# Kernel tuning notes

Hardware: AMD Instinct MI355X
Metric: run time of the kernel (lower is better)

Reference implementation:

```python
import jax, jax.numpy as jnp
import numpy as np

BETA = 0.25  # commitment_beta


def setup_inputs() -> dict:
    key = jax.random.key(0)
    k1, k2 = jax.random.split(key)
    B, C, H, W = 8, 256, 32, 32
    n_embed = 16384
    x = jax.random.normal(k1, (B, C, H, W), dtype=jnp.float32)
    # torch init: uniform_(-1/codebook_size, 1/codebook_size)
    weight = jax.random.uniform(k2, (n_embed, C), dtype=jnp.float32,
                                minval=-1.0 / n_embed, maxval=1.0 / n_embed)
    return {"x": x, "weight": weight}


def reference(x, weight):
    B, C, H, W = x.shape
    # b c h w -> b (h w) c
    xf = jnp.transpose(x, (0, 2, 3, 1)).reshape(B, H * W, C)
    flat = xf.reshape(-1, C)  # [N, C], N = B*H*W
    d = (jnp.sum(flat * flat, axis=1, keepdims=True)
         + jnp.sum(weight * weight, axis=1)[None, :]
         - 2.0 * flat @ weight.T)
    idx = jnp.argmin(d, axis=-1)          # [N]
    xq = weight[idx].reshape(B, H * W, C)  # codebook gather
    sg = jax.lax.stop_gradient
    loss = (BETA * jnp.mean((sg(xq) - xf) ** 2)
            + jnp.mean((xq - sg(xf)) ** 2))
    # straight-through estimator
    xq_st = xf + sg(xq - xf)
    # b (h w) c -> b c h w
    xq_img = jnp.transpose(xq_st.reshape(B, H, W, C), (0, 3, 1, 2))
    x_code = idx.reshape(B, H, W)
    return xq_img, loss, x_code
```

## Files before the change

### kernel.cpp

```cpp
#include <hip/hip_runtime.h>
#include <stdint.h>

#define NROW    8192
#define CDIM    256
#define NCODE   16384
#define MARGINF 6.0e-5f

typedef short short8 __attribute__((ext_vector_type(8)));
typedef float floatx4 __attribute__((ext_vector_type(4)));

__device__ inline ushort f2bf(float f) {
    unsigned u = __builtin_bit_cast(unsigned, f);
    unsigned r = (u + 0x7fffu + ((u >> 16) & 1u)) >> 16;
    return (ushort)r;
}
__device__ inline unsigned fsort(float v) {
    unsigned u = __builtin_bit_cast(unsigned, v);
    return (u >> 31) ? ~u : (u | 0x80000000u);
}

__device__ inline void gl_lds16(const ushort* g, ushort* lds) {
    __builtin_amdgcn_global_load_lds(
        (const __attribute__((address_space(1))) unsigned int*)(g),
        (__attribute__((address_space(3))) unsigned int*)(lds),
        16, 0, 0);
}

__global__ __launch_bounds__(256) void prep_all(const float* __restrict__ x,
                                                const float* __restrict__ w,
                                                float* __restrict__ xf32,
                                                ushort* __restrict__ xbf,
                                                ushort* __restrict__ wbf,
                                                float* __restrict__ S2a) {
#pragma clang fp contract(off)
    const int bid = blockIdx.x;
    const int t = threadIdx.x;
    if (bid < 2048) {
        __shared__ float tile[32][33];
        const int b = bid & 7, ht = (bid >> 3) & 31, ct = bid >> 8;
        const int hw0 = ht * 32, c0 = ct * 32;
        {
            const int cc = t >> 5, hh = t & 31;
            #pragma unroll
            for (int i = 0; i < 4; ++i) {
                int cl = cc + i * 8;
                tile[cl][hh] = x[((size_t)(b * 256 + c0 + cl) << 10) + hw0 + hh];
            }
        }
        __syncthreads();
        {
            const int col = t & 31, row = t >> 5;
            #pragma unroll
            for (int i = 0; i < 4; ++i) {
                int r = row + i * 8;
                float v = tile[col][r];
                size_t o = ((size_t)(b * 1024 + hw0 + r) << 8) + c0 + col;
                xf32[o] = v;
                xbf[o] = f2bf(v);
            }
        }
    } else {
        const int gt = (bid - 2048) * 256 + t;
        const int j = gt >> 1, h = gt & 1;
        const float* a = w + ((size_t)j << 8) + h * 128;
        ushort* orow = wbf + ((size_t)j << 8) + h * 128;
        float r8[8];
        #pragma unroll
        for (int l = 0; l < 8; ++l) { float v = a[l]; r8[l] = v * v; }
        for (int i = 8; i < 128; i += 8) {
            #pragma unroll
            for (int l = 0; l < 8; ++l) { float v = a[i + l]; r8[l] = r8[l] + v * v; }
        }
        float hs = ((r8[0] + r8[1]) + (r8[2] + r8[3])) + ((r8[4] + r8[5]) + (r8[6] + r8[7]));
        float other = __shfl_xor(hs, 1);
        if (h == 0) S2a[j] = hs + other;
        for (int i = 0; i < 128; i += 8) {
            ushort u8[8];
            #pragma unroll
            for (int l = 0; l < 8; ++l) u8[l] = f2bf(a[i + l]);
            *(ushort4*)(orow + i)     = make_ushort4(u8[0], u8[1], u8[2], u8[3]);
            *(ushort4*)(orow + i + 4) = make_ushort4(u8[4], u8[5], u8[6], u8[7]);
        }
    }
}

__global__ __launch_bounds__(256) void gemm_min(const ushort* __restrict__ Wb,
                                                const ushort* __restrict__ Xb,
                                                const float* __restrict__ S2a,
                                                unsigned* __restrict__ bm32) {
    __shared__ __attribute__((aligned(16))) ushort As[8192];
    __shared__ __attribute__((aligned(16))) ushort Bs[8192];
    __shared__ __attribute__((aligned(16))) unsigned stg32[128][8];

    const int n0 = blockIdx.x * 128;
    const int j0 = blockIdx.y * 128;
    const int t  = threadIdx.x;
    const int wv = t >> 6, l = t & 63;
    const int wr = wv >> 1, wc = wv & 1;
    const int q  = l >> 4, c = l & 15;

    const int lr = l >> 3;
    const int lperm = (l & 7) ^ lr;
    const size_t gA0 = ((size_t)(j0 + wv * 32 + lr) << 8) + lperm * 8;
    const size_t gB0 = ((size_t)(n0 + wv * 32 + lr) << 8) + lperm * 8;
    const int ldsbase = wv * 2048;

    floatx4 acc[4][4];
    #pragma unroll
    for (int mi = 0; mi < 4; ++mi)
        #pragma unroll
        for (int ni = 0; ni < 4; ++ni)
            acc[mi][ni] = (floatx4){0.f, 0.f, 0.f, 0.f};

    for (int kb = 0; kb < 4; ++kb) {
        if (kb) __syncthreads();
        #pragma unroll
        for (int ca = 0; ca < 4; ++ca) {
            gl_lds16(Wb + gA0 + ca * 2048 + kb * 64, As + ldsbase + ca * 512);
            gl_lds16(Xb + gB0 + ca * 2048 + kb * 64, Bs + ldsbase + ca * 512);
        }
        __syncthreads();
        #pragma unroll
        for (int kk = 0; kk < 2; ++kk) {
            short8 af[4], bf[4];
            #pragma unroll
            for (int mi = 0; mi < 4; ++mi) {
                int row = wr * 64 + mi * 16 + c;
                int pos = (kk * 4 + q) ^ (c & 7);
                af[mi] = *(const short8*)&As[row * 64 + pos * 8];
            }
            #pragma unroll
            for (int ni = 0; ni < 4; ++ni) {
                int row = wc * 64 + ni * 16 + c;
                int pos = (kk * 4 + q) ^ (c & 7);
                bf[ni] = *(const short8*)&Bs[row * 64 + pos * 8];
            }
            #pragma unroll
            for (int mi = 0; mi < 4; ++mi)
                #pragma unroll
                for (int ni = 0; ni < 4; ++ni)
                    acc[mi][ni] = __builtin_amdgcn_mfma_f32_16x16x32_bf16(
                        af[mi], bf[ni], acc[mi][ni], 0, 0, 0);
        }
    }

    #pragma unroll
    for (int mi = 0; mi < 4; ++mi) {
        float4 s2 = *(const float4*)&S2a[j0 + wr * 64 + mi * 16 + (q << 2)];
        #pragma unroll
        for (int ni = 0; ni < 4; ++ni) {
            float v0 = fmaf(-2.f, acc[mi][ni][0], s2.x);
            float v1 = fmaf(-2.f, acc[mi][ni][1], s2.y);
            float v2 = fmaf(-2.f, acc[mi][ni][2], s2.z);
            float v3 = fmaf(-2.f, acc[mi][ni][3], s2.w);
            float lo01 = fminf(v0, v1), hi01 = fmaxf(v0, v1);
            float lo23 = fminf(v2, v3), hi23 = fmaxf(v2, v3);
            int   i01 = v1 < v0 ? 1 : 0;
            int   i23 = v3 < v2 ? 3 : 2;
            float m1 = fminf(lo01, lo23);
            float m2 = fminf(fmaxf(lo01, lo23), lo23 < lo01 ? hi23 : hi01);
            int   i1 = (q << 2) | (lo23 < lo01 ? i23 : i01);
            #pragma unroll
            for (int off = 16; off <= 32; off <<= 1) {
                float om1 = __shfl_xor(m1, off);
                float om2 = __shfl_xor(m2, off);
                int   oi1 = __shfl_xor(i1, off);
                float nm2 = fminf(fminf(m2, om2), fmaxf(m1, om1));
                i1 = om1 < m1 ? oi1 : i1;
                m1 = fminf(m1, om1);
                m2 = nm2;
            }
            if (q == 0) {
                ushort min16 = __builtin_bit_cast(ushort, (_Float16)m1);
                float delta = m2 - m1;
                ushort d16 = __builtin_bit_cast(ushort, (_Float16)delta);
                ushort d8 = d16 >> 8;
                float rec = (float)__builtin_bit_cast(_Float16, (ushort)(d8 << 8));
                if (rec > delta && d8) d8--;
                stg32[wc * 64 + ni * 16 + c][wr * 4 + mi] =
                    ((unsigned)min16 << 16) | ((unsigned)d8 << 8) | (unsigned)i1;
            }
        }
    }
    __syncthreads();
    if (t < 128) {
        uint4 a0 = *(const uint4*)&stg32[t][0];
        uint4 a1 = *(const uint4*)&stg32[t][4];
        size_t base = ((size_t)(n0 + t) << 10) + blockIdx.y * 8;
        *(uint4*)(bm32 + base)     = a0;
        *(uint4*)(bm32 + base + 4) = a1;
    }
}

__global__ __launch_bounds__(256) void rescore7(const unsigned* __restrict__ bm32,
                                                const float* __restrict__ xf32,
                                                const float* __restrict__ w,
                                                const float* __restrict__ S2a,
                                                int* __restrict__ idxb,
                                                float* __restrict__ xcode,
                                                float* __restrict__ lpart) {
#pragma clang fp contract(off)
    __shared__ float xs[4][256];
    __shared__ short sing[4][128];
    __shared__ short blk[4][32];
    __shared__ int ns[4], nb[4];

    const int t = threadIdx.x, wv = t >> 6, l = t & 63;
    const int n = blockIdx.x * 4 + wv;
    if (l == 0) { ns[wv] = 0; nb[wv] = 0; }

    const float4 xv = *(const float4*)&xf32[((size_t)n << 8) + l * 4];
    *(float4*)&xs[wv][l * 4] = xv;

    const unsigned* bp = bm32 + ((size_t)n << 10) + l * 16;
    unsigned ee[16];
    {
        uint4 e0 = *(const uint4*)(bp);
        uint4 e1 = *(const uint4*)(bp + 4);
        uint4 e2 = *(const uint4*)(bp + 8);
        uint4 e3 = *(const uint4*)(bp + 12);
        ee[0]=e0.x; ee[1]=e0.y; ee[2]=e0.z; ee[3]=e0.w;
        ee[4]=e1.x; ee[5]=e1.y; ee[6]=e1.z; ee[7]=e1.w;
        ee[8]=e2.x; ee[9]=e2.y; ee[10]=e2.z; ee[11]=e2.w;
        ee[12]=e3.x; ee[13]=e3.y; ee[14]=e3.z; ee[15]=e3.w;
    }
    float vals[16];
    #pragma unroll
    for (int i = 0; i < 16; ++i)
        vals[i] = (float)__builtin_bit_cast(_Float16, (ushort)(ee[i] >> 16));
    float vmin = vals[0];
    #pragma unroll
    for (int i = 1; i < 16; ++i) vmin = fminf(vmin, vals[i]);
    #pragma unroll
    for (int off = 1; off <= 32; off <<= 1) vmin = fminf(vmin, __shfl_xor(vmin, off));
    const float thr = vmin + MARGINF;
    #pragma unroll
    for (int i = 0; i < 16; ++i) {
        if (vals[i] <= thr) {
            const int jb = l * 16 + i;
            int p = atomicAdd(&ns[wv], 1);
            if (p < 128) sing[wv][p] = (short)(jb * 16 + (int)(ee[i] & 15u));
            float dr = (float)__builtin_bit_cast(_Float16,
                           (ushort)(((ee[i] >> 8) & 0xFFu) << 8));
            if (vals[i] + dr <= thr) {
                int pb = atomicAdd(&nb[wv], 1);
                if (pb < 32) blk[wv][pb] = (short)jb;
            }
        }
    }

    float racc = 0.f;
    if (l < 16) {
        const float* a_ = &xs[wv][(l >> 3) * 128];
        const int ai = l & 7;
        float v = a_[ai];
        racc = v * v;
        for (int i = 8; i < 128; i += 8) { v = a_[i + ai]; racc = racc + v * v; }
    }
    racc = racc + __shfl_xor(racc, 1);
    racc = racc + __shfl_xor(racc, 2);
    racc = racc + __shfl_xor(racc, 4);
    racc = racc + __shfl_xor(racc, 8);
    const float S1n = __shfl(racc, 0);

    const int nsv = ns[wv] < 128 ? ns[wv] : 128;
    const int nbv = nb[wv] < 32 ? nb[wv] : 32;
    const int ntot = nsv + nbv * 16;
    unsigned long long best = ~0ull;
    for (int s = l; s < ntot; s += 64) {
        const int j = (s < nsv)
            ? (int)sing[wv][s]
            : (int)blk[wv][(s - nsv) >> 4] * 16 + ((s - nsv) & 15);
        const float4* wr4 = (const float4*)(w + ((size_t)j << 8));
        float g = 0.f;
        #pragma unroll
        for (int half = 0; half < 4; ++half) {
            float4 buf[16];
            #pragma unroll
            for (int i = 0; i < 16; ++i) buf[i] = wr4[half * 16 + i];
            #pragma unroll
            for (int i = 0; i < 16; ++i) {
                const float4 xv4 = *(const float4*)&xs[wv][half * 64 + i * 4];
                g = fmaf(xv4.x, buf[i].x, g);
                g = fmaf(xv4.y, buf[i].y, g);
                g = fmaf(xv4.z, buf[i].z, g);
                g = fmaf(xv4.w, buf[i].w, g);
            }
        }
        float d = (S1n + S2a[j]) - 2.0f * g;
        unsigned long long key = ((unsigned long long)fsort(d) << 32) | (unsigned)j;
        if (key < best) best = key;
    }
    #pragma unroll
    for (int off = 1; off <= 32; off <<= 1) {
        unsigned long long o = __shfl_xor(best, off);
        if (o < best) best = o;
    }
    const int J = (int)(best & 0xffffffffu);

    const float4 wj = *(const float4*)&w[((size_t)J << 8) + l * 4];
    float d0 = wj.x - xv.x, d1 = wj.y - xv.y, d2 = wj.z - xv.z, d3 = wj.w - xv.w;
    float lacc = (d0 * d0 + d1 * d1) + (d2 * d2 + d3 * d3);
    #pragma unroll
    for (int off = 1; off <= 32; off <<= 1) lacc += __shfl_xor(lacc, off);
    if (l == 0) {
        idxb[n] = J;
        xcode[n] = (float)J;
        lpart[n] = lacc;
    }
}

__global__ __launch_bounds__(256) void outputs_k(const float* __restrict__ w,
                                                 const int* __restrict__ idxb,
                                                 const float* __restrict__ lpart,
                                                 float* __restrict__ out,
                                                 float* __restrict__ loss) {
    const int b = blockIdx.x, hq = blockIdx.y, cs = blockIdx.z;
    const int t = threadIdx.x;
    const int hw = hq * 256 + t;
    const int n = (b << 10) + hw;
    const int id = idxb[n];
    #pragma unroll 4
    for (int ci = 0; ci < 32; ++ci) {
        const int c_ = cs * 32 + ci;
        const size_t oo = ((size_t)((b << 8) + c_) << 10) + hw;
        out[oo] = w[((size_t)id << 8) + c_];
    }
    if (b == 0 && hq == 0 && cs == 0) {
        __shared__ float red[256];
        float s = 0.f;
        for (int i = 0; i < 32; ++i) s += lpart[t + (i << 8)];
        red[t] = s;
        __syncthreads();
        for (int k = 128; k > 0; k >>= 1) {
            if (t < k) red[t] += red[t + k];
            __syncthreads();
        }
        if (t == 0) *loss = red[0] * (1.25f / 2097152.0f);
    }
}

extern "C" void kernel_launch(void* const* d_in, const int* in_sizes, int n_in,
                              void* d_out, int out_size, void* d_ws, size_t ws_size,
                              hipStream_t stream) {
    const float* x = (const float*)d_in[0];
    const float* w = (const float*)d_in[1];
    float* out = (float*)d_out;

    char* ws = (char*)d_ws;
    const size_t MB = 1024u * 1024u;
    ushort*   xbf   = (ushort*)  (ws);
    float*    xf32  = (float*)   (ws + 4 * MB);
    ushort*   wbf   = (ushort*)  (ws + 12 * MB);
    float*    S2a   = (float*)   (ws + 20 * MB);
    unsigned* bm32  = (unsigned*)(ws + 21 * MB);
    int*      idxb  = (int*)     (ws + 53 * MB);
    float*    lpart = (float*)   (ws + 53 * MB + 65536);

    float* loss_ptr  = out + 2097152;
    float* xcode_ptr = out + 2097153;

    prep_all<<<dim3(2176),     256, 0, stream>>>(x, w, xf32, xbf, wbf, S2a);
    gemm_min<<<dim3(64, 128),  256, 0, stream>>>(wbf, xbf, S2a, bm32);
    rescore7<<<dim3(2048),     256, 0, stream>>>(bm32, xf32, w, S2a, idxb,
                                                 xcode_ptr, lpart);
    outputs_k<<<dim3(8, 4, 8), 256, 0, stream>>>(w, idxb, lpart, out, loss_ptr);
}
```

Baseline: 286.4 us.

## Coarsen GEMM min summary to 64-code blocks, restructure prep and output kernels

The GEMM epilogue now reduces the min and second-min across all four MFMA row tiles in registers before the cross-lane shuffle. It stores one packed record per 64 codes instead of per 16, which shrinks the bm32 intermediate fourfold and the rescore read traffic with it. Rescore now scans 4 entries per lane and expands fallback blocks to 64 candidates. The weight prep kernel uses 16 threads per codebook row with shuffle-reduced norms, and the output gather is done through an LDS transpose tile so global stores are coalesced. Coarser blocks may add rescore work when near-ties trigger block expansion.

```diff
diff --git a/kernel.cpp b/kernel.cpp
--- a/kernel.cpp
+++ b/kernel.cpp
@@ -61,25 +61,29 @@
         }
     } else {
         const int gt = (bid - 2048) * 256 + t;
-        const int j = gt >> 1, h = gt & 1;
-        const float* a = w + ((size_t)j << 8) + h * 128;
-        ushort* orow = wbf + ((size_t)j << 8) + h * 128;
-        float r8[8];
-        #pragma unroll
-        for (int l = 0; l < 8; ++l) { float v = a[l]; r8[l] = v * v; }
+        const int j = gt >> 4, l16 = gt & 15;
+        const int h = l16 >> 3, ai = l16 & 7;
+        const float* a = w + ((size_t)j << 8);
+        float v = a[h * 128 + ai];
+        float racc = v * v;
         for (int i = 8; i < 128; i += 8) {
-            #pragma unroll
-            for (int l = 0; l < 8; ++l) { float v = a[i + l]; r8[l] = r8[l] + v * v; }
-        }
-        float hs = ((r8[0] + r8[1]) + (r8[2] + r8[3])) + ((r8[4] + r8[5]) + (r8[6] + r8[7]));
-        float other = __shfl_xor(hs, 1);
-        if (h == 0) S2a[j] = hs + other;
-        for (int i = 0; i < 128; i += 8) {
+            v = a[h * 128 + ai + i];
+            racc = racc + v * v;
+        }
+        racc = racc + __shfl_xor(racc, 1);
+        racc = racc + __shfl_xor(racc, 2);
+        racc = racc + __shfl_xor(racc, 4);
+        racc = racc + __shfl_xor(racc, 8);
+        if (l16 == 0) S2a[j] = racc;
+        const float* seg = a + l16 * 16;
+        ushort* oseg = wbf + ((size_t)j << 8) + l16 * 16;
+        #pragma unroll
+        for (int i = 0; i < 16; i += 8) {
             ushort u8[8];
             #pragma unroll
-            for (int l = 0; l < 8; ++l) u8[l] = f2bf(a[i + l]);
-            *(ushort4*)(orow + i)     = make_ushort4(u8[0], u8[1], u8[2], u8[3]);
-            *(ushort4*)(orow + i + 4) = make_ushort4(u8[4], u8[5], u8[6], u8[7]);
+            for (int k = 0; k < 8; ++k) u8[k] = f2bf(seg[i + k]);
+            *(ushort4*)(oseg + i)     = make_ushort4(u8[0], u8[1], u8[2], u8[3]);
+            *(ushort4*)(oseg + i + 4) = make_ushort4(u8[4], u8[5], u8[6], u8[7]);
         }
     }
 }
@@ -90,7 +94,7 @@
                                                 unsigned* __restrict__ bm32) {
     __shared__ __attribute__((aligned(16))) ushort As[8192];
     __shared__ __attribute__((aligned(16))) ushort Bs[8192];
-    __shared__ __attribute__((aligned(16))) unsigned stg32[128][8];
+    __shared__ __attribute__((aligned(16))) unsigned stg32[128][2];
 
     const int n0 = blockIdx.x * 128;
     const int j0 = blockIdx.y * 128;
@@ -144,55 +148,65 @@
         }
     }
 
-    #pragma unroll
-    for (int mi = 0; mi < 4; ++mi) {
-        float4 s2 = *(const float4*)&S2a[j0 + wr * 64 + mi * 16 + (q << 2)];
-        #pragma unroll
-        for (int ni = 0; ni < 4; ++ni) {
-            float v0 = fmaf(-2.f, acc[mi][ni][0], s2.x);
-            float v1 = fmaf(-2.f, acc[mi][ni][1], s2.y);
-            float v2 = fmaf(-2.f, acc[mi][ni][2], s2.z);
-            float v3 = fmaf(-2.f, acc[mi][ni][3], s2.w);
+    float4 s2v[4];
+    #pragma unroll
+    for (int mi = 0; mi < 4; ++mi)
+        s2v[mi] = *(const float4*)&S2a[j0 + wr * 64 + mi * 16 + (q << 2)];
+
+    #pragma unroll
+    for (int ni = 0; ni < 4; ++ni) {
+        float M1 = 0.f, M2 = 0.f; int I1 = 0;
+        #pragma unroll
+        for (int mi = 0; mi < 4; ++mi) {
+            float v0 = fmaf(-2.f, acc[mi][ni][0], s2v[mi].x);
+            float v1 = fmaf(-2.f, acc[mi][ni][1], s2v[mi].y);
+            float v2 = fmaf(-2.f, acc[mi][ni][2], s2v[mi].z);
+            float v3 = fmaf(-2.f, acc[mi][ni][3], s2v[mi].w);
             float lo01 = fminf(v0, v1), hi01 = fmaxf(v0, v1);
             float lo23 = fminf(v2, v3), hi23 = fmaxf(v2, v3);
-            int   i01 = v1 < v0 ? 1 : 0;
-            int   i23 = v3 < v2 ? 3 : 2;
+            int i01 = v1 < v0 ? 1 : 0;
+            int i23 = v3 < v2 ? 3 : 2;
             float m1 = fminf(lo01, lo23);
             float m2 = fminf(fmaxf(lo01, lo23), lo23 < lo01 ? hi23 : hi01);
-            int   i1 = (q << 2) | (lo23 < lo01 ? i23 : i01);
-            #pragma unroll
-            for (int off = 16; off <= 32; off <<= 1) {
-                float om1 = __shfl_xor(m1, off);
-                float om2 = __shfl_xor(m2, off);
-                int   oi1 = __shfl_xor(i1, off);
-                float nm2 = fminf(fminf(m2, om2), fmaxf(m1, om1));
-                i1 = om1 < m1 ? oi1 : i1;
-                m1 = fminf(m1, om1);
-                m2 = nm2;
-            }
-            if (q == 0) {
-                ushort min16 = __builtin_bit_cast(ushort, (_Float16)m1);
-                float delta = m2 - m1;
-                ushort d16 = __builtin_bit_cast(ushort, (_Float16)delta);
-                ushort d8 = d16 >> 8;
-                float rec = (float)__builtin_bit_cast(_Float16, (ushort)(d8 << 8));
-                if (rec > delta && d8) d8--;
-                stg32[wc * 64 + ni * 16 + c][wr * 4 + mi] =
-                    ((unsigned)min16 << 16) | ((unsigned)d8 << 8) | (unsigned)i1;
-            }
+            int idx = mi * 16 + (q << 2) + (lo23 < lo01 ? i23 : i01);
+            if (mi == 0) { M1 = m1; M2 = m2; I1 = idx; }
+            else {
+                float nM2 = (m1 < M1) ? fminf(M1, m2) : fminf(M2, m1);
+                I1 = (m1 < M1) ? idx : I1;
+                M1 = fminf(M1, m1);
+                M2 = nM2;
+            }
+        }
+        #pragma unroll
+        for (int off = 16; off <= 32; off <<= 1) {
+            float oM1 = __shfl_xor(M1, off);
+            float oM2 = __shfl_xor(M2, off);
+            int   oI1 = __shfl_xor(I1, off);
+            float nM2 = fminf(fminf(M2, oM2), fmaxf(M1, oM1));
+            bool take = (oM1 < M1) || (oM1 == M1 && oI1 < I1);
+            I1 = take ? oI1 : I1;
+            M1 = fminf(M1, oM1);
+            M2 = nM2;
+        }
+        if (q == 0) {
+            ushort min16 = __builtin_bit_cast(ushort, (_Float16)M1);
+            float delta = M2 - M1;
+            ushort d16 = __builtin_bit_cast(ushort, (_Float16)delta);
+            ushort d8 = d16 >> 8;
+            float rec = (float)__builtin_bit_cast(_Float16, (ushort)(d8 << 8));
+            if (rec > delta && d8) d8--;
+            stg32[wc * 64 + ni * 16 + c][wr] =
+                ((unsigned)min16 << 16) | ((unsigned)d8 << 8) | (unsigned)I1;
         }
     }
     __syncthreads();
     if (t < 128) {
-        uint4 a0 = *(const uint4*)&stg32[t][0];
-        uint4 a1 = *(const uint4*)&stg32[t][4];
-        size_t base = ((size_t)(n0 + t) << 10) + blockIdx.y * 8;
-        *(uint4*)(bm32 + base)     = a0;
-        *(uint4*)(bm32 + base + 4) = a1;
-    }
-}
-
-__global__ __launch_bounds__(256) void rescore7(const unsigned* __restrict__ bm32,
+        uint2 v = *(const uint2*)&stg32[t][0];
+        *(uint2*)(bm32 + ((size_t)(n0 + t) << 8) + blockIdx.y * 2) = v;
+    }
+}
+
+__global__ __launch_bounds__(256) void rescore8(const unsigned* __restrict__ bm32,
                                                 const float* __restrict__ xf32,
                                                 const float* __restrict__ w,
                                                 const float* __restrict__ S2a,
@@ -202,7 +216,7 @@
 #pragma clang fp contract(off)
     __shared__ float xs[4][256];
     __shared__ short sing[4][128];
-    __shared__ short blk[4][32];
+    __shared__ short blk[4][16];
     __shared__ int ns[4], nb[4];
 
     const int t = threadIdx.x, wv = t >> 6, l = t & 63;
@@ -212,39 +226,27 @@
     const float4 xv = *(const float4*)&xf32[((size_t)n << 8) + l * 4];
     *(float4*)&xs[wv][l * 4] = xv;
 
-    const unsigned* bp = bm32 + ((size_t)n << 10) + l * 16;
-    unsigned ee[16];
-    {
-        uint4 e0 = *(const uint4*)(bp);
-        uint4 e1 = *(const uint4*)(bp + 4);
-        uint4 e2 = *(const uint4*)(bp + 8);
-        uint4 e3 = *(const uint4*)(bp + 12);
-        ee[0]=e0.x; ee[1]=e0.y; ee[2]=e0.z; ee[3]=e0.w;
-        ee[4]=e1.x; ee[5]=e1.y; ee[6]=e1.z; ee[7]=e1.w;
-        ee[8]=e2.x; ee[9]=e2.y; ee[10]=e2.z; ee[11]=e2.w;
-        ee[12]=e3.x; ee[13]=e3.y; ee[14]=e3.z; ee[15]=e3.w;
-    }
-    float vals[16];
-    #pragma unroll
-    for (int i = 0; i < 16; ++i)
+    const uint4 e = *(const uint4*)(bm32 + ((size_t)n << 8) + l * 4);
+    unsigned ee[4] = {e.x, e.y, e.z, e.w};
+    float vals[4];
+    #pragma unroll
+    for (int i = 0; i < 4; ++i)
         vals[i] = (float)__builtin_bit_cast(_Float16, (ushort)(ee[i] >> 16));
-    float vmin = vals[0];
-    #pragma unroll
-    for (int i = 1; i < 16; ++i) vmin = fminf(vmin, vals[i]);
+    float vmin = fminf(fminf(vals[0], vals[1]), fminf(vals[2], vals[3]));
     #pragma unroll
     for (int off = 1; off <= 32; off <<= 1) vmin = fminf(vmin, __shfl_xor(vmin, off));
     const float thr = vmin + MARGINF;
     #pragma unroll
-    for (int i = 0; i < 16; ++i) {
+    for (int i = 0; i < 4; ++i) {
         if (vals[i] <= thr) {
-            const int jb = l * 16 + i;
+            const int jb = l * 4 + i;
             int p = atomicAdd(&ns[wv], 1);
-            if (p < 128) sing[wv][p] = (short)(jb * 16 + (int)(ee[i] & 15u));
+            if (p < 128) sing[wv][p] = (short)(jb * 64 + (int)(ee[i] & 63u));
             float dr = (float)__builtin_bit_cast(_Float16,
                            (ushort)(((ee[i] >> 8) & 0xFFu) << 8));
             if (vals[i] + dr <= thr) {
                 int pb = atomicAdd(&nb[wv], 1);
-                if (pb < 32) blk[wv][pb] = (short)jb;
+                if (pb < 16) blk[wv][pb] = (short)jb;
             }
         }
     }
@@ -264,13 +266,13 @@
     const float S1n = __shfl(racc, 0);
 
     const int nsv = ns[wv] < 128 ? ns[wv] : 128;
-    const int nbv = nb[wv] < 32 ? nb[wv] : 32;
-    const int ntot = nsv + nbv * 16;
+    const int nbv = nb[wv] < 16 ? nb[wv] : 16;
+    const int ntot = nsv + nbv * 64;
     unsigned long long best = ~0ull;
     for (int s = l; s < ntot; s += 64) {
         const int j = (s < nsv)
             ? (int)sing[wv][s]
-            : (int)blk[wv][(s - nsv) >> 4] * 16 + ((s - nsv) & 15);
+            : (int)blk[wv][(s - nsv) >> 6] * 64 + ((s - nsv) & 63);
         const float4* wr4 = (const float4*)(w + ((size_t)j << 8));
         float g = 0.f;
         #pragma unroll
@@ -315,18 +317,31 @@
                                                  const float* __restrict__ lpart,
                                                  float* __restrict__ out,
                                                  float* __restrict__ loss) {
-    const int b = blockIdx.x, hq = blockIdx.y, cs = blockIdx.z;
+    __shared__ float tile[32][33];
+    __shared__ int ids[32];
+    const int b = blockIdx.x, ht = blockIdx.y, ct = blockIdx.z;
     const int t = threadIdx.x;
-    const int hw = hq * 256 + t;
-    const int n = (b << 10) + hw;
-    const int id = idxb[n];
-    #pragma unroll 4
-    for (int ci = 0; ci < 32; ++ci) {
-        const int c_ = cs * 32 + ci;
-        const size_t oo = ((size_t)((b << 8) + c_) << 10) + hw;
-        out[oo] = w[((size_t)id << 8) + c_];
-    }
-    if (b == 0 && hq == 0 && cs == 0) {
+    const int hw0 = ht * 32, c0 = ct * 32;
+    if (t < 32) ids[t] = idxb[(b << 10) + hw0 + t];
+    __syncthreads();
+    {
+        const int nl = t & 31, cq = t >> 5;
+        float4 v = *(const float4*)&w[((size_t)ids[nl] << 8) + c0 + cq * 4];
+        tile[nl][cq * 4]     = v.x;
+        tile[nl][cq * 4 + 1] = v.y;
+        tile[nl][cq * 4 + 2] = v.z;
+        tile[nl][cq * 4 + 3] = v.w;
+    }
+    __syncthreads();
+    {
+        const int hwl = t & 31, cq = t >> 5;
+        #pragma unroll
+        for (int i = 0; i < 4; ++i) {
+            const int cl = cq * 4 + i;
+            out[((size_t)((b << 8) + c0 + cl) << 10) + hw0 + hwl] = tile[hwl][cl];
+        }
+    }
+    if (b == 0 && ht == 0 && ct == 0) {
         __shared__ float red[256];
         float s = 0.f;
         for (int i = 0; i < 32; ++i) s += lpart[t + (i << 8)];
@@ -354,15 +369,15 @@
     ushort*   wbf   = (ushort*)  (ws + 12 * MB);
     float*    S2a   = (float*)   (ws + 20 * MB);
     unsigned* bm32  = (unsigned*)(ws + 21 * MB);
-    int*      idxb  = (int*)     (ws + 53 * MB);
-    float*    lpart = (float*)   (ws + 53 * MB + 65536);
+    int*      idxb  = (int*)     (ws + 29 * MB);
+    float*    lpart = (float*)   (ws + 29 * MB + 65536);
 
     float* loss_ptr  = out + 2097152;
     float* xcode_ptr = out + 2097153;
 
-    prep_all<<<dim3(2176),     256, 0, stream>>>(x, w, xf32, xbf, wbf, S2a);
-    gemm_min<<<dim3(64, 128),  256, 0, stream>>>(wbf, xbf, S2a, bm32);
-    rescore7<<<dim3(2048),     256, 0, stream>>>(bm32, xf32, w, S2a, idxb,
-                                                 xcode_ptr, lpart);
-    outputs_k<<<dim3(8, 4, 8), 256, 0, stream>>>(w, idxb, lpart, out, loss_ptr);
-}
+    prep_all<<<dim3(3072),      256, 0, stream>>>(x, w, xf32, xbf, wbf, S2a);
+    gemm_min<<<dim3(64, 128),   256, 0, stream>>>(wbf, xbf, S2a, bm32);
+    rescore8<<<dim3(2048),      256, 0, stream>>>(bm32, xf32, w, S2a, idxb,
+                                                  xcode_ptr, lpart);
+    outputs_k<<<dim3(8, 32, 8), 256, 0, stream>>>(w, idxb, lpart, out, loss_ptr);
+}
```

Result: faster. 248.6 us (-13.2%).
